# Performance work log

Hardware: AMD Instinct MI355X
Metric: run time of the kernel (lower is better)

Reference implementation:

```python
import jax, jax.numpy as jnp
import numpy as np

HEAD_DIM = 128
MEM_SIZE = 512
MEM_COMPRESS = 256   # mem_size * (1 - hh_keep_rate)
KEEP_HH = 256        # mem_size - mem_compress
LOCAL_LEN = 64


def setup_inputs() -> dict:
    key = jax.random.key(0)
    ks = jax.random.split(key, 8)
    b, h, s, d = 2, 32, 8192, HEAD_DIM
    return dict(
        past_key_states=jax.random.normal(ks[0], (b, h, s, d), jnp.float32),
        past_value_states=jax.random.normal(ks[1], (b, h, s, d), jnp.float32),
        hh_scores=jax.random.uniform(ks[2], (b, h, s), jnp.float32),
        conv0_w=jax.random.normal(ks[3], (2 * MEM_COMPRESS, 2 * HEAD_DIM, 3), jnp.float32) * 0.02,
        conv0_b=jax.random.normal(ks[4], (2 * MEM_COMPRESS,), jnp.float32) * 0.02,
        conv1_w=jax.random.normal(ks[5], (MEM_COMPRESS, 2 * MEM_COMPRESS, 3), jnp.float32) * 0.02,
        conv1_b=jax.random.normal(ks[6], (MEM_COMPRESS,), jnp.float32) * 0.02,
        normalizer=jnp.ones((1,), jnp.float32) * 0.5,
    )


def _conv1d(x, w, bias):
    # x: [N, C_in, L], w: [C_out, C_in, K], 'same' padding for K=3
    y = jax.lax.conv_general_dilated(x, w, window_strides=(1,), padding=[(1, 1)],
                                     dimension_numbers=('NCH', 'OIH', 'NCH'))
    return y + bias[None, :, None]


def reference(past_key_states, past_value_states, hh_scores,
              conv0_w, conv0_b, conv1_w, conv1_b, normalizer):
    b, h, s, d = past_key_states.shape
    # ---- partition_past_key_values: topk + scatter mask, then ordered gather
    k_top = KEEP_HH - LOCAL_LEN
    _, hh_idxs = jax.lax.top_k(hh_scores[..., : s - LOCAL_LEN], k_top)  # [b,h,k_top]
    mask = jnp.zeros((b, h, s), dtype=bool)
    bi = jnp.arange(b)[:, None, None]
    hi = jnp.arange(h)[None, :, None]
    mask = mask.at[bi, hi, hh_idxs].set(True)
    mask = mask.at[..., -LOCAL_LEN:].set(True)
    # stable argsort of ~mask puts mask-True positions first, each group in
    # original sequence order == torch.masked_select ordering
    order = jnp.argsort(~mask, axis=-1, stable=True)          # [b,h,s]
    hh_pos = order[..., :KEEP_HH]                              # [b,h,KEEP_HH]
    non_pos = order[..., KEEP_HH:]                             # [b,h,s-KEEP_HH]
    hh_k = jnp.take_along_axis(past_key_states, hh_pos[..., None], axis=2)
    hh_v = jnp.take_along_axis(past_value_states, hh_pos[..., None], axis=2)
    non_k = jnp.take_along_axis(past_key_states, non_pos[..., None], axis=2)
    non_v = jnp.take_along_axis(past_value_states, non_pos[..., None], axis=2)
    non_scores = jnp.take_along_axis(hh_scores, non_pos, axis=-1)  # [b,h,S']
    sp = s - KEEP_HH
    # ---- make_residual_weight: topk -> sorted idx -> scatter ones
    _, ridx = jax.lax.top_k(non_scores, MEM_COMPRESS)
    ridx = jnp.sort(ridx, axis=-1)
    residual = jax.nn.one_hot(ridx, sp, dtype=past_key_states.dtype)  # [b,h,M,S']
    # ---- conv stack over concatenated (K,V) channels
    x = jnp.concatenate([non_k, non_v], axis=-1)               # [b,h,S',2d]
    x = x.transpose(0, 1, 3, 2).reshape(b * h, 2 * d, sp)      # [(b h), 2d, S']
    x = jax.nn.silu(_conv1d(x, conv0_w, conv0_b))
    x = jax.nn.silu(_conv1d(x, conv1_w, conv1_b))              # [(b h), M, S']
    w = jax.nn.softmax(x, axis=-1).reshape(b, h, MEM_COMPRESS, sp)
    w = residual * (1.0 - normalizer) + w * normalizer         # normalizer: [1]
    merged_k = jnp.einsum('bhms,bhsd->bhmd', w, non_k)
    merged_v = jnp.einsum('bhms,bhsd->bhmd', w, non_v)
    keys = jnp.concatenate([hh_k, merged_k], axis=2)           # [b,h,mem_size,d]
    vals = jnp.concatenate([hh_v, merged_v], axis=2)
    return (keys, vals)
```

## Files before the change

### kernel.cpp

```cpp
#include <hip/hip_runtime.h>
#include <stdint.h>

#define BB 2
#define HH 32
#define NBH 64
#define S 8192
#define DD 128
#define SP 7936
#define MC 256
#define KEEP 256
#define LOC 64
#define KTOP 192
#define N1 8128
#define OC0 512
#define IC0 256
#define KK0 768
#define OC1 256
#define IC1 512
#define KK1 1536
#define KEYS_TOTAL ((size_t)NBH * 512 * DD)

typedef unsigned short u16;
typedef __attribute__((ext_vector_type(2))) unsigned short us2;
typedef __attribute__((ext_vector_type(4))) unsigned short us4;
typedef __attribute__((ext_vector_type(8))) unsigned short us8;
typedef __attribute__((ext_vector_type(8))) short bfrag;
typedef __attribute__((ext_vector_type(4))) float ffrag;

__device__ __forceinline__ u16 f2bf(float x) {
  uint32_t u = __float_as_uint(x);
  return (u16)((u + 0x7FFFu + ((u >> 16) & 1u)) >> 16);
}
__device__ __forceinline__ float bf2f(u16 h) {
  return __uint_as_float(((uint32_t)h) << 16);
}

__device__ __forceinline__ void gl_lds16(const u16* g, u16* l) {
  __builtin_amdgcn_global_load_lds(
      (const __attribute__((address_space(1))) void*)g,
      (__attribute__((address_space(3))) void*)l,
      16, 0, 0);
}

__global__ __launch_bounds__(256) void sel_kernel(
    const float* __restrict__ scores, int bh0,
    int* __restrict__ non_pos_g, int* __restrict__ hh_pos_g, int* __restrict__ rpos_g,
    float* __restrict__ sums_g)
{
  __shared__ uint32_t keys[N1];
  __shared__ u16 nonpos_l[SP];
  __shared__ uint32_t hist[256];
  __shared__ int scanb[256];
  __shared__ uint32_t s_pref, s_pmask;
  __shared__ int s_krem;

  const int slot = blockIdx.x;
  const int bh = bh0 + slot;
  const int tid = threadIdx.x;
  const float* row = scores + (size_t)bh * S;

  sums_g[slot * MC + tid] = 0.0f;

  for (int i = tid; i < N1; i += 256) {
    uint32_t u = __float_as_uint(row[i]);
    keys[i] = (u >> 31) ? ~u : (u | 0x80000000u);
  }
  __syncthreads();

  if (tid == 0) { s_pref = 0; s_pmask = 0; s_krem = KTOP; }
  __syncthreads();
  for (int shift = 24; shift >= 0; shift -= 8) {
    hist[tid] = 0; __syncthreads();
    uint32_t pm = s_pmask, pf = s_pref;
    for (int i = tid; i < N1; i += 256) {
      uint32_t u = keys[i];
      if ((u & pm) == pf) atomicAdd(&hist[(u >> shift) & 255u], 1u);
    }
    __syncthreads();
    if (tid == 0) {
      int krem = s_krem, c = 0, chosen = 0;
      for (int b = 255; b >= 0; --b) {
        int h = (int)hist[b];
        if (krem <= c + h) { chosen = b; krem -= c; break; }
        c += h;
      }
      s_pref |= ((uint32_t)chosen) << shift;
      s_pmask |= 255u << shift;
      s_krem = krem;
    }
    __syncthreads();
  }
  const uint32_t T1 = s_pref;
  const int need1 = s_krem;

  const int base = tid * 32;
  int eqc = 0;
  for (int j = 0; j < 32; ++j) { int i = base + j; if (i < N1 && keys[i] == T1) ++eqc; }
  __syncthreads(); scanb[tid] = eqc; __syncthreads();
  if (tid == 0) { int run = 0; for (int t = 0; t < 256; ++t) { int v = scanb[t]; scanb[t] = run; run += v; } }
  __syncthreads();
  const int eqb = scanb[tid];

  int mcnt = 0;
  { int er = eqb;
    for (int j = 0; j < 32; ++j) {
      int i = base + j; bool m;
      if (i >= N1) m = true;
      else { uint32_t u = keys[i];
        if (u > T1) m = true; else if (u == T1) { m = (er < need1); ++er; } else m = false; }
      if (m) ++mcnt;
    } }
  __syncthreads(); scanb[tid] = mcnt; __syncthreads();
  if (tid == 0) { int run = 0; for (int t = 0; t < 256; ++t) { int v = scanb[t]; scanb[t] = run; run += v; } }
  __syncthreads();
  { int mo = scanb[tid];
    int no = base - mo;
    int er = eqb;
    for (int j = 0; j < 32; ++j) {
      int i = base + j; bool m;
      if (i >= N1) m = true;
      else { uint32_t u = keys[i];
        if (u > T1) m = true; else if (u == T1) { m = (er < need1); ++er; } else m = false; }
      if (m) { hh_pos_g[slot * KEEP + mo] = i; ++mo; }
      else   { nonpos_l[no] = (u16)i; non_pos_g[(size_t)slot * SP + no] = i; ++no; }
    } }
  __syncthreads();

  if (tid == 0) { s_pref = 0; s_pmask = 0; s_krem = MC; }
  __syncthreads();
  for (int shift = 24; shift >= 0; shift -= 8) {
    hist[tid] = 0; __syncthreads();
    uint32_t pm = s_pmask, pf = s_pref;
    for (int i = tid; i < SP; i += 256) {
      uint32_t u = keys[nonpos_l[i]];
      if ((u & pm) == pf) atomicAdd(&hist[(u >> shift) & 255u], 1u);
    }
    __syncthreads();
    if (tid == 0) {
      int krem = s_krem, c = 0, chosen = 0;
      for (int b = 255; b >= 0; --b) {
        int h = (int)hist[b];
        if (krem <= c + h) { chosen = b; krem -= c; break; }
        c += h;
      }
      s_pref |= ((uint32_t)chosen) << shift;
      s_pmask |= 255u << shift;
      s_krem = krem;
    }
    __syncthreads();
  }
  const uint32_t T2 = s_pref;
  const int need2 = s_krem;
  const int b2 = tid * 31;
  int eqc2 = 0;
  for (int j = 0; j < 31; ++j) { if (keys[nonpos_l[b2 + j]] == T2) ++eqc2; }
  __syncthreads(); scanb[tid] = eqc2; __syncthreads();
  if (tid == 0) { int run = 0; for (int t = 0; t < 256; ++t) { int v = scanb[t]; scanb[t] = run; run += v; } }
  __syncthreads();
  const int eqb2 = scanb[tid];
  int sc = 0;
  { int er = eqb2;
    for (int j = 0; j < 31; ++j) {
      uint32_t u = keys[nonpos_l[b2 + j]]; bool sel;
      if (u > T2) sel = true; else if (u == T2) { sel = (er < need2); ++er; } else sel = false;
      if (sel) ++sc;
    } }
  __syncthreads(); scanb[tid] = sc; __syncthreads();
  if (tid == 0) { int run = 0; for (int t = 0; t < 256; ++t) { int v = scanb[t]; scanb[t] = run; run += v; } }
  __syncthreads();
  { int so = scanb[tid];
    int er = eqb2;
    for (int j = 0; j < 31; ++j) {
      int i = b2 + j; uint32_t u = keys[nonpos_l[i]]; bool sel;
      if (u > T2) sel = true; else if (u == T2) { sel = (er < need2); ++er; } else sel = false;
      if (sel) { rpos_g[slot * MC + so] = (int)nonpos_l[i]; ++so; }
    } }
}

__global__ __launch_bounds__(256) void gather_kernel(
    const float* __restrict__ pk, const float* __restrict__ pv,
    const int* __restrict__ non_pos, u16* __restrict__ Xtm_all,
    u16* __restrict__ Xdm_all, u16* __restrict__ Y0_all, int bh0)
{
  __shared__ u16 lt[256][66];
  const int slot = blockIdx.y, tile = blockIdx.x;
  const int bh = bh0 + slot;
  const int tid = threadIdx.x, lane = tid & 63, q = tid >> 6;
  const int t0 = tile * 64;
  u16* Xtm = Xtm_all + (size_t)slot * (SP + 2) * 256 + 256;
  const int* np = non_pos + (size_t)slot * SP;

  for (int r = q; r < 64; r += 4) {
    const int t = t0 + r;
    const int pos = np[t];
    float2 kk = ((const float2*)(pk + ((size_t)bh * S + pos) * DD))[lane];
    float2 vv = ((const float2*)(pv + ((size_t)bh * S + pos) * DD))[lane];
    u16 k0 = f2bf(kk.x), k1 = f2bf(kk.y), v0 = f2bf(vv.x), v1 = f2bf(vv.y);
    us2 tk = {k0, k1}; us2 tv = {v0, v1};
    *(us2*)&Xtm[(size_t)t * 256 + lane * 2] = tk;
    *(us2*)&Xtm[(size_t)t * 256 + 128 + lane * 2] = tv;
    lt[lane * 2][r] = k0; lt[lane * 2 + 1][r] = k1;
    lt[128 + lane * 2][r] = v0; lt[128 + lane * 2 + 1][r] = v1;
  }
  if (tile == 0) {
    Xtm[-256 + tid] = 0;
    u16* y0 = Y0_all + (size_t)slot * (SP + 2) * 512;
    y0[tid] = 0; y0[tid + 256] = 0;
  } else if (tile == 123) {
    Xtm[(size_t)SP * 256 + tid] = 0;
    u16* y0 = Y0_all + (size_t)slot * (SP + 2) * 512 + (size_t)(SP + 1) * 512;
    y0[tid] = 0; y0[tid + 256] = 0;
  }
  __syncthreads();
  u16* Xdm = Xdm_all + (size_t)slot * 256 * SP;
  for (int idx = tid; idx < 4096; idx += 256) {
    const int r = idx >> 4, j = idx & 15;
    uint2 v = *(const uint2*)&lt[r][j * 4];
    *(uint2*)(Xdm + (size_t)r * SP + t0 + j * 4) = v;
  }
}

__global__ __launch_bounds__(256) void hhgather_kernel(
    const float* __restrict__ pk, const float* __restrict__ pv,
    const int* __restrict__ hh_pos, float* __restrict__ out, int bh0)
{
  const int slot = blockIdx.y, bh = bh0 + slot;
  const int tid = threadIdx.x, lane = tid & 63, q = tid >> 6;
  const int r0 = blockIdx.x * 16;
  const int* hp = hh_pos + slot * KEEP;
  for (int r = r0 + q; r < r0 + 16; r += 4) {
    const int pos = hp[r];
    float2 kk = ((const float2*)(pk + ((size_t)bh * S + pos) * DD))[lane];
    float2 vv = ((const float2*)(pv + ((size_t)bh * S + pos) * DD))[lane];
    ((float2*)(out + ((size_t)bh * 512 + r) * DD))[lane] = kk;
    ((float2*)(out + KEYS_TOTAL + ((size_t)bh * 512 + r) * DD))[lane] = vv;
  }
}

__global__ __launch_bounds__(256) void prepack_kernel(
    const float* __restrict__ w0, const float* __restrict__ w1,
    u16* __restrict__ A0, u16* __restrict__ A1)
{
  const int idx = blockIdx.x * 256 + threadIdx.x;
  if (idx < OC0 * KK0) {
    int oc = idx / KK0, r = idx % KK0, tau = r / IC0, ic = r % IC0;
    A0[idx] = f2bf(w0[(oc * IC0 + ic) * 3 + tau]);
  }
  if (idx < OC1 * KK1) {
    int oc = idx / KK1, r = idx % KK1, tau = r / IC1, ic = r % IC1;
    A1[idx] = f2bf(w1[(oc * IC1 + ic) * 3 + tau]);
  }
}

template<int MTOT, int KTOT, int TAUCH, int OUTMODE>
__global__ __launch_bounds__(256) void conv_gemm_kernel(
    const u16* __restrict__ Apack, const u16* __restrict__ Bsrc_all,
    const float* __restrict__ bias, u16* __restrict__ out_all,
    float* __restrict__ sums_g)
{
  __shared__ u16 smem[128 * 136];
  __shared__ float rowsum[128];
  u16* Asl = smem;
  u16* Bsl = smem + 4096;
  const int slot = blockIdx.z;
  const int m0 = blockIdx.y * 128;
  const int t0 = blockIdx.x * 128;
  const int tid = threadIdx.x;
  const int lane = tid & 63, wave = tid >> 6;
  const int wm = (wave & 1) * 64, wn = (wave >> 1) * 64;
  const int r_fr = lane & 15, quad = lane >> 4;
  const u16* Bsrc = Bsrc_all + (size_t)slot * (size_t)(SP + 2) * TAUCH + TAUCH;

  ffrag acc[4][4];
  #pragma unroll
  for (int a = 0; a < 4; ++a)
    #pragma unroll
    for (int b = 0; b < 4; ++b) acc[a][b] = (ffrag)0.0f;

  const int c0 = wave * 2;
  const int lrow = lane >> 2, lcol = (lane & 3) * 8;
  const u16* gA0 = Apack + (size_t)(m0 + c0 * 16 + lrow) * KTOT + lcol;
  const u16* gA1 = gA0 + (size_t)16 * KTOT;
  const u16* gB0 = Bsrc + ((long)t0 + c0 * 16 + lrow - 1) * (long)TAUCH + lcol;
  const u16* gB1 = gB0 + (size_t)16 * TAUCH;
  u16* lA = Asl + c0 * 512;
  u16* lB = Bsl + c0 * 512;

  for (int kt = 0; kt < KTOT / 32; ++kt) {
    const int ko = kt * 32;
    __syncthreads();
    gl_lds16(gA0 + ko, lA);
    gl_lds16(gA1 + ko, lA + 512);
    gl_lds16(gB0 + ko, lB);
    gl_lds16(gB1 + ko, lB + 512);
    __syncthreads();
    bfrag af[4], bf[4];
    #pragma unroll
    for (int mt = 0; mt < 4; ++mt)
      af[mt] = *(const bfrag*)&Asl[(wm + mt * 16 + r_fr) * 32 + quad * 8];
    #pragma unroll
    for (int nt = 0; nt < 4; ++nt)
      bf[nt] = *(const bfrag*)&Bsl[(wn + nt * 16 + r_fr) * 32 + quad * 8];
    #pragma unroll
    for (int mt = 0; mt < 4; ++mt)
      #pragma unroll
      for (int nt = 0; nt < 4; ++nt)
        acc[mt][nt] = __builtin_amdgcn_mfma_f32_16x16x32_bf16(af[mt], bf[nt], acc[mt][nt], 0, 0, 0);
  }
  __syncthreads();
  if constexpr (OUTMODE == 1) {
    if (tid < 128) rowsum[tid] = 0.0f;
    __syncthreads();
  }

  #pragma unroll
  for (int mt = 0; mt < 4; ++mt) {
    float srow4[4] = {0.0f, 0.0f, 0.0f, 0.0f};
    #pragma unroll
    for (int nt = 0; nt < 4; ++nt) {
      const int n_l = wn + nt * 16 + r_fr;
      const int m_l = wm + mt * 16 + quad * 4;
      if constexpr (OUTMODE == 0) {
        u16 h4[4];
        #pragma unroll
        for (int r = 0; r < 4; ++r) {
          float x = acc[mt][nt][r] + bias[m0 + m_l + r];
          float y = x / (1.0f + __expf(-x));
          h4[r] = f2bf(y);
        }
        us4 p = {h4[0], h4[1], h4[2], h4[3]};
        *(us4*)&smem[n_l * 136 + m_l] = p;
      } else {
        #pragma unroll
        for (int r = 0; r < 4; ++r) {
          float x = acc[mt][nt][r] + bias[m0 + m_l + r];
          float y = x / (1.0f + __expf(-x));
          float p = __expf(fminf(y, 60.0f));
          srow4[r] += p;
          smem[(m_l + r) * 136 + n_l] = f2bf(p);
        }
      }
    }
    if constexpr (OUTMODE == 1) {
      #pragma unroll
      for (int r = 0; r < 4; ++r) {
        float s = srow4[r];
        s += __shfl_xor(s, 1, 64);
        s += __shfl_xor(s, 2, 64);
        s += __shfl_xor(s, 4, 64);
        s += __shfl_xor(s, 8, 64);
        if ((lane & 15) == 0)
          atomicAdd(&rowsum[wm + mt * 16 + quad * 4 + r], s);
      }
    }
  }
  __syncthreads();
  if constexpr (OUTMODE == 1) {
    if (tid < 128) atomicAdd(&sums_g[slot * MC + m0 + tid], rowsum[tid]);
  }
  const int rr = tid >> 1, half = tid & 1;
  if (OUTMODE == 0) {
    u16* orow = out_all + (size_t)slot * (size_t)(SP + 2) * MTOT + MTOT
              + (size_t)(t0 + rr) * MTOT + m0 + half * 64;
    const u16* srcr = &smem[rr * 136 + half * 64];
    #pragma unroll
    for (int j = 0; j < 8; ++j) *(us8*)(orow + j * 8) = *(const us8*)(srcr + j * 8);
  } else {
    u16* orow = out_all + (size_t)slot * (size_t)MC * SP
              + (size_t)(m0 + rr) * SP + t0 + half * 64;
    const u16* srcr = &smem[rr * 136 + half * 64];
    #pragma unroll
    for (int j = 0; j < 8; ++j) *(us8*)(orow + j * 8) = *(const us8*)(srcr + j * 8);
  }
}

__global__ __launch_bounds__(256) void gemm3_kernel(
    const u16* __restrict__ Wmm_all, const u16* __restrict__ Xdm_all,
    float* __restrict__ part)
{
  __shared__ u16 smem[8192];
  u16* Asl = smem;
  u16* Bsl = smem + 4096;
  const int kc = blockIdx.x;
  const int tile = blockIdx.y;
  const int slot = blockIdx.z;
  const int m0 = (tile >> 1) * 128, n0 = (tile & 1) * 128;
  const int tid = threadIdx.x;
  const int lane = tid & 63, wave = tid >> 6;
  const int wm = (wave & 1) * 64, wn = (wave >> 1) * 64;
  const int r_fr = lane & 15, quad = lane >> 4;
  const u16* A = Wmm_all + (size_t)slot * MC * SP;
  const u16* Bt = Xdm_all + (size_t)slot * 256 * SP;
  const int kbeg = kc * (SP / 4);

  ffrag acc[4][4];
  #pragma unroll
  for (int a = 0; a < 4; ++a)
    #pragma unroll
    for (int b = 0; b < 4; ++b) acc[a][b] = (ffrag)0.0f;

  const int c0 = wave * 2;
  const int lrow = lane >> 2, lcol = (lane & 3) * 8;
  const u16* gA0 = A + (size_t)(m0 + c0 * 16 + lrow) * SP + kbeg + lcol;
  const u16* gA1 = gA0 + (size_t)16 * SP;
  const u16* gB0 = Bt + (size_t)(n0 + c0 * 16 + lrow) * SP + kbeg + lcol;
  const u16* gB1 = gB0 + (size_t)16 * SP;
  u16* lA = Asl + c0 * 512;
  u16* lB = Bsl + c0 * 512;

  for (int kt = 0; kt < (SP / 4) / 32; ++kt) {
    const int ko = kt * 32;
    __syncthreads();
    gl_lds16(gA0 + ko, lA);
    gl_lds16(gA1 + ko, lA + 512);
    gl_lds16(gB0 + ko, lB);
    gl_lds16(gB1 + ko, lB + 512);
    __syncthreads();
    bfrag af[4], bf[4];
    #pragma unroll
    for (int mt = 0; mt < 4; ++mt)
      af[mt] = *(const bfrag*)&Asl[(wm + mt * 16 + r_fr) * 32 + quad * 8];
    #pragma unroll
    for (int nt = 0; nt < 4; ++nt)
      bf[nt] = *(const bfrag*)&Bsl[(wn + nt * 16 + r_fr) * 32 + quad * 8];
    #pragma unroll
    for (int mt = 0; mt < 4; ++mt)
      #pragma unroll
      for (int nt = 0; nt < 4; ++nt)
        acc[mt][nt] = __builtin_amdgcn_mfma_f32_16x16x32_bf16(af[mt], bf[nt], acc[mt][nt], 0, 0, 0);
  }
  float* pbase = part + ((size_t)slot * 4 + kc) * MC * 256;
  #pragma unroll
  for (int mt = 0; mt < 4; ++mt)
    #pragma unroll
    for (int nt = 0; nt < 4; ++nt) {
      const int n_l = wn + nt * 16 + r_fr;
      const int m_l = wm + mt * 16 + quad * 4;
      #pragma unroll
      for (int r = 0; r < 4; ++r)
        pbase[(size_t)(m0 + m_l + r) * 256 + n0 + n_l] = acc[mt][nt][r];
    }
}

__global__ __launch_bounds__(256) void combine_kernel(
    const float* __restrict__ part, const float* __restrict__ pk, const float* __restrict__ pv,
    const int* __restrict__ rpos, const float* __restrict__ nrmp,
    const float* __restrict__ sums_g, float* __restrict__ out, int bh0)
{
  const int slot = blockIdx.y;
  const int m = blockIdx.x * 4 + (threadIdx.x >> 6);
  const int lane = threadIdx.x & 63;
  const int bh = bh0 + slot;
  const float nrm = nrmp[0];
  const float rw = 1.0f - nrm;
  const float scale = nrm / sums_g[slot * MC + m];
  const int pos = rpos[slot * MC + m];
  const float* krow = pk + ((size_t)bh * S + pos) * DD;
  const float* vrow = pv + ((size_t)bh * S + pos) * DD;
  const size_t pb = (size_t)slot * 4 * MC * 256;
  #pragma unroll
  for (int h = 0; h < 2; ++h) {
    const int d = lane + h * 64;
    float sk = 0.0f, sv = 0.0f;
    #pragma unroll
    for (int kcc = 0; kcc < 4; ++kcc) {
      const float* pp = part + pb + (size_t)kcc * MC * 256 + (size_t)m * 256;
      sk += pp[d];
      sv += pp[128 + d];
    }
    sk = sk * scale + rw * krow[d];
    sv = sv * scale + rw * vrow[d];
    out[((size_t)bh * 512 + KEEP + m) * DD + d] = sk;
    out[KEYS_TOTAL + ((size_t)bh * 512 + KEEP + m) * DD + d] = sv;
  }
}

extern "C" void kernel_launch(void* const* d_in, const int* in_sizes, int n_in,
                              void* d_out, int out_size, void* d_ws, size_t ws_size,
                              hipStream_t stream)
{
  (void)in_sizes; (void)n_in; (void)out_size;
  const float* pk = (const float*)d_in[0];
  const float* pv = (const float*)d_in[1];
  const float* scores = (const float*)d_in[2];
  const float* w0 = (const float*)d_in[3];
  const float* b0 = (const float*)d_in[4];
  const float* w1 = (const float*)d_in[5];
  const float* b1 = (const float*)d_in[6];
  const float* nrmp = (const float*)d_in[7];
  float* out = (float*)d_out;
  char* ws = (char*)d_ws;

  auto alignup = [](size_t x) { return (x + 255) & ~(size_t)255; };
  const size_t offA0 = 0;
  const size_t offA1 = alignup(offA0 + (size_t)OC0 * KK0 * 2);
  const size_t fixed_end = alignup(offA1 + (size_t)OC1 * KK1 * 2);

  const size_t sz_np = (size_t)SP * 4;
  const size_t sz_hh = (size_t)KEEP * 4;
  const size_t sz_rp = (size_t)MC * 4;
  const size_t sz_sm = (size_t)MC * 4;
  const size_t sz_xtm = (size_t)(SP + 2) * 256 * 2;
  const size_t sz_xdm = (size_t)256 * SP * 2;
  const size_t sz_y0 = (size_t)(SP + 2) * 512 * 2;
  const size_t sz_w = (size_t)MC * SP * 2;
  const size_t sz_part = (size_t)4 * MC * 256 * 4;

  auto need_for = [&](int g) -> size_t {
    size_t o = fixed_end;
    o = alignup(o + (size_t)g * sz_np);
    o = alignup(o + (size_t)g * sz_hh);
    o = alignup(o + (size_t)g * sz_rp);
    o = alignup(o + (size_t)g * sz_sm);
    o = alignup(o + (size_t)g * sz_xtm);
    o = alignup(o + (size_t)g * sz_xdm);
    o = alignup(o + (size_t)g * sz_y0);
    o = alignup(o + (size_t)g * sz_w);
    o = alignup(o + (size_t)g * sz_part);
    return o;
  };
  int G = 1;
  const int cand[7] = {64, 32, 16, 8, 4, 2, 1};
  for (int ci = 0; ci < 7; ++ci) { if (need_for(cand[ci]) <= ws_size) { G = cand[ci]; break; } }

  size_t o = fixed_end;
  const size_t off_np = o;  o = alignup(o + (size_t)G * sz_np);
  const size_t off_hh = o;  o = alignup(o + (size_t)G * sz_hh);
  const size_t off_rp = o;  o = alignup(o + (size_t)G * sz_rp);
  const size_t off_sm = o;  o = alignup(o + (size_t)G * sz_sm);
  const size_t off_xtm = o; o = alignup(o + (size_t)G * sz_xtm);
  const size_t off_xdm = o; o = alignup(o + (size_t)G * sz_xdm);
  const size_t off_y0 = o;  o = alignup(o + (size_t)G * sz_y0);
  const size_t off_w = o;   o = alignup(o + (size_t)G * sz_w);
  const size_t off_part = o;

  u16* A0 = (u16*)(ws + offA0);
  u16* A1 = (u16*)(ws + offA1);
  int* np_p = (int*)(ws + off_np);
  int* hh_p = (int*)(ws + off_hh);
  int* rp_p = (int*)(ws + off_rp);
  float* sums = (float*)(ws + off_sm);
  u16* Xtm = (u16*)(ws + off_xtm);
  u16* Xdm = (u16*)(ws + off_xdm);
  u16* Y0 = (u16*)(ws + off_y0);
  u16* Wmm = (u16*)(ws + off_w);
  float* part = (float*)(ws + off_part);

  prepack_kernel<<<1536, 256, 0, stream>>>(w0, w1, A0, A1);

  for (int bh0 = 0; bh0 < NBH; bh0 += G) {
    sel_kernel<<<G, 256, 0, stream>>>(scores, bh0, np_p, hh_p, rp_p, sums);
    gather_kernel<<<dim3(124, G), 256, 0, stream>>>(pk, pv, np_p, Xtm, Xdm, Y0, bh0);
    hhgather_kernel<<<dim3(16, G), 256, 0, stream>>>(pk, pv, hh_p, out, bh0);
    conv_gemm_kernel<OC0, KK0, 256, 0><<<dim3(62, 4, G), 256, 0, stream>>>(A0, Xtm, b0, Y0, sums);
    conv_gemm_kernel<OC1, KK1, 512, 1><<<dim3(62, 2, G), 256, 0, stream>>>(A1, Y0, b1, Wmm, sums);
    gemm3_kernel<<<dim3(4, 4, G), 256, 0, stream>>>(Wmm, Xdm, part);
    combine_kernel<<<dim3(64, G), 256, 0, stream>>>(part, pk, pv, rp_p, nrmp, sums, out, bh0);
  }
}
```

Before: 2.393 ms.

## Double-buffer LDS tiles in conv and gemm3 kernels and remap blocks across XCDs

Both GEMM-style kernels now use two LDS buffers, so the global-to-LDS load for the next K-step is issued before the MFMA work on the current step, and each K-step needs one barrier instead of two. The conv kernels also flatten the grid to 1D and remap block indices so consecutive tiles that share A/B data land on the same XCD, aiming at better L2 reuse. This costs twice the LDS staging in gemm3 and may reduce occupancy there. It relies on NK being even for the paired-loop structure.

```diff
diff --git a/kernel.cpp b/kernel.cpp
--- a/kernel.cpp
+++ b/kernel.cpp
@@ -258,13 +258,22 @@
     const float* __restrict__ bias, u16* __restrict__ out_all,
     float* __restrict__ sums_g)
 {
+  constexpr int MTILES = MTOT / 128;
+  constexpr int NK = KTOT / 32;
+  constexpr int NX = (SP / 128) * MTILES;
+  constexpr int QX = NX / 8, RX = NX % 8;
   __shared__ u16 smem[128 * 136];
   __shared__ float rowsum[128];
-  u16* Asl = smem;
-  u16* Bsl = smem + 4096;
-  const int slot = blockIdx.z;
-  const int m0 = blockIdx.y * 128;
-  const int t0 = blockIdx.x * 128;
+  u16* A0l = smem;
+  u16* A1l = smem + 4096;
+  u16* B0l = smem + 8192;
+  u16* B1l = smem + 12288;
+  const int slot = blockIdx.y;
+  const int lin = blockIdx.x;
+  const int xcd = lin & 7, pos = lin >> 3;
+  const int widx = (xcd < RX ? xcd * (QX + 1) : RX * (QX + 1) + (xcd - RX) * QX) + pos;
+  const int m0 = (widx % MTILES) * 128;
+  const int t0 = (widx / MTILES) * 128;
   const int tid = threadIdx.x;
   const int lane = tid & 63, wave = tid >> 6;
   const int wm = (wave & 1) * 64, wn = (wave >> 1) * 64;
@@ -283,17 +292,10 @@
   const u16* gA1 = gA0 + (size_t)16 * KTOT;
   const u16* gB0 = Bsrc + ((long)t0 + c0 * 16 + lrow - 1) * (long)TAUCH + lcol;
   const u16* gB1 = gB0 + (size_t)16 * TAUCH;
-  u16* lA = Asl + c0 * 512;
-  u16* lB = Bsl + c0 * 512;
-
-  for (int kt = 0; kt < KTOT / 32; ++kt) {
-    const int ko = kt * 32;
-    __syncthreads();
-    gl_lds16(gA0 + ko, lA);
-    gl_lds16(gA1 + ko, lA + 512);
-    gl_lds16(gB0 + ko, lB);
-    gl_lds16(gB1 + ko, lB + 512);
-    __syncthreads();
+  u16* lA0 = A0l + c0 * 512; u16* lA1 = A1l + c0 * 512;
+  u16* lB0 = B0l + c0 * 512; u16* lB1 = B1l + c0 * 512;
+
+  auto compute = [&](const u16* Asl, const u16* Bsl) {
     bfrag af[4], bf[4];
     #pragma unroll
     for (int mt = 0; mt < 4; ++mt)
@@ -306,8 +308,29 @@
       #pragma unroll
       for (int nt = 0; nt < 4; ++nt)
         acc[mt][nt] = __builtin_amdgcn_mfma_f32_16x16x32_bf16(af[mt], bf[nt], acc[mt][nt], 0, 0, 0);
-  }
-  __syncthreads();
+  };
+
+  gl_lds16(gA0, lA0); gl_lds16(gA1, lA0 + 512);
+  gl_lds16(gB0, lB0); gl_lds16(gB1, lB0 + 512);
+  __syncthreads();
+
+  for (int kp = 0; kp < NK / 2; ++kp) {
+    {
+      const int ko = (2 * kp + 1) * 32;
+      gl_lds16(gA0 + ko, lA1); gl_lds16(gA1 + ko, lA1 + 512);
+      gl_lds16(gB0 + ko, lB1); gl_lds16(gB1 + ko, lB1 + 512);
+    }
+    compute(A0l, B0l);
+    __syncthreads();
+    if (2 * kp + 2 < NK) {
+      const int ko = (2 * kp + 2) * 32;
+      gl_lds16(gA0 + ko, lA0); gl_lds16(gA1 + ko, lA0 + 512);
+      gl_lds16(gB0 + ko, lB0); gl_lds16(gB1 + ko, lB0 + 512);
+    }
+    compute(A1l, B1l);
+    __syncthreads();
+  }
+
   if constexpr (OUTMODE == 1) {
     if (tid < 128) rowsum[tid] = 0.0f;
     __syncthreads();
@@ -378,9 +401,11 @@
     const u16* __restrict__ Wmm_all, const u16* __restrict__ Xdm_all,
     float* __restrict__ part)
 {
-  __shared__ u16 smem[8192];
-  u16* Asl = smem;
-  u16* Bsl = smem + 4096;
+  __shared__ u16 smem[16384];
+  u16* A0l = smem;
+  u16* A1l = smem + 4096;
+  u16* B0l = smem + 8192;
+  u16* B1l = smem + 12288;
   const int kc = blockIdx.x;
   const int tile = blockIdx.y;
   const int slot = blockIdx.z;
@@ -392,6 +417,7 @@
   const u16* A = Wmm_all + (size_t)slot * MC * SP;
   const u16* Bt = Xdm_all + (size_t)slot * 256 * SP;
   const int kbeg = kc * (SP / 4);
+  constexpr int NK = (SP / 4) / 32;
 
   ffrag acc[4][4];
   #pragma unroll
@@ -405,17 +431,10 @@
   const u16* gA1 = gA0 + (size_t)16 * SP;
   const u16* gB0 = Bt + (size_t)(n0 + c0 * 16 + lrow) * SP + kbeg + lcol;
   const u16* gB1 = gB0 + (size_t)16 * SP;
-  u16* lA = Asl + c0 * 512;
-  u16* lB = Bsl + c0 * 512;
-
-  for (int kt = 0; kt < (SP / 4) / 32; ++kt) {
-    const int ko = kt * 32;
-    __syncthreads();
-    gl_lds16(gA0 + ko, lA);
-    gl_lds16(gA1 + ko, lA + 512);
-    gl_lds16(gB0 + ko, lB);
-    gl_lds16(gB1 + ko, lB + 512);
-    __syncthreads();
+  u16* lA0 = A0l + c0 * 512; u16* lA1 = A1l + c0 * 512;
+  u16* lB0 = B0l + c0 * 512; u16* lB1 = B1l + c0 * 512;
+
+  auto compute = [&](const u16* Asl, const u16* Bsl) {
     bfrag af[4], bf[4];
     #pragma unroll
     for (int mt = 0; mt < 4; ++mt)
@@ -428,7 +447,29 @@
       #pragma unroll
       for (int nt = 0; nt < 4; ++nt)
         acc[mt][nt] = __builtin_amdgcn_mfma_f32_16x16x32_bf16(af[mt], bf[nt], acc[mt][nt], 0, 0, 0);
-  }
+  };
+
+  gl_lds16(gA0, lA0); gl_lds16(gA1, lA0 + 512);
+  gl_lds16(gB0, lB0); gl_lds16(gB1, lB0 + 512);
+  __syncthreads();
+
+  for (int kp = 0; kp < NK / 2; ++kp) {
+    {
+      const int ko = (2 * kp + 1) * 32;
+      gl_lds16(gA0 + ko, lA1); gl_lds16(gA1 + ko, lA1 + 512);
+      gl_lds16(gB0 + ko, lB1); gl_lds16(gB1 + ko, lB1 + 512);
+    }
+    compute(A0l, B0l);
+    __syncthreads();
+    if (2 * kp + 2 < NK) {
+      const int ko = (2 * kp + 2) * 32;
+      gl_lds16(gA0 + ko, lA0); gl_lds16(gA1 + ko, lA0 + 512);
+      gl_lds16(gB0 + ko, lB0); gl_lds16(gB1 + ko, lB0 + 512);
+    }
+    compute(A1l, B1l);
+    __syncthreads();
+  }
+
   float* pbase = part + ((size_t)slot * 4 + kc) * MC * 256;
   #pragma unroll
   for (int mt = 0; mt < 4; ++mt)
@@ -552,8 +593,8 @@
     sel_kernel<<<G, 256, 0, stream>>>(scores, bh0, np_p, hh_p, rp_p, sums);
     gather_kernel<<<dim3(124, G), 256, 0, stream>>>(pk, pv, np_p, Xtm, Xdm, Y0, bh0);
     hhgather_kernel<<<dim3(16, G), 256, 0, stream>>>(pk, pv, hh_p, out, bh0);
-    conv_gemm_kernel<OC0, KK0, 256, 0><<<dim3(62, 4, G), 256, 0, stream>>>(A0, Xtm, b0, Y0, sums);
-    conv_gemm_kernel<OC1, KK1, 512, 1><<<dim3(62, 2, G), 256, 0, stream>>>(A1, Y0, b1, Wmm, sums);
+    conv_gemm_kernel<OC0, KK0, 256, 0><<<dim3(248, G), 256, 0, stream>>>(A0, Xtm, b0, Y0, sums);
+    conv_gemm_kernel<OC1, KK1, 512, 1><<<dim3(124, G), 256, 0, stream>>>(A1, Y0, b1, Wmm, sums);
     gemm3_kernel<<<dim3(4, 4, G), 256, 0, stream>>>(Wmm, Xdm, part);
     combine_kernel<<<dim3(64, G), 256, 0, stream>>>(part, pk, pv, rp_p, nrmp, sums, out, bh0);
   }
```

Measured after the change: 2.481 ms. 1.04x slower.

## Double K-step per barrier and remap conv GEMM blocks for XCD locality

Applied to the files above, without the earlier changes.

The conv GEMM and gemm3 kernels now load a 64-wide K slice per iteration (two 32-wide halves in LDS), which halves the number of syncthreads barriers per unit of MFMA work. The conv GEMM grid is also flattened and remapped so that consecutive tiles, which share the same time range and M tiles, land on the same XCD under round-robin dispatch, improving L2 reuse of the B operand. LDS use doubles for these tiles, which may lower occupancy.

```diff
diff --git a/kernel.cpp b/kernel.cpp
--- a/kernel.cpp
+++ b/kernel.cpp
@@ -258,13 +258,20 @@
     const float* __restrict__ bias, u16* __restrict__ out_all,
     float* __restrict__ sums_g)
 {
+  constexpr int MTILES = MTOT / 128;
+  constexpr int NK = KTOT / 64;
+  constexpr int NX = (SP / 128) * MTILES;
+  constexpr int QX = NX / 8, RX = NX % 8;
   __shared__ u16 smem[128 * 136];
   __shared__ float rowsum[128];
   u16* Asl = smem;
-  u16* Bsl = smem + 4096;
-  const int slot = blockIdx.z;
-  const int m0 = blockIdx.y * 128;
-  const int t0 = blockIdx.x * 128;
+  u16* Bsl = smem + 8192;
+  const int slot = blockIdx.y;
+  const int lin = blockIdx.x;
+  const int xcd = lin & 7, pos = lin >> 3;
+  const int widx = (xcd < RX ? xcd * (QX + 1) : RX * (QX + 1) + (xcd - RX) * QX) + pos;
+  const int m0 = (widx % MTILES) * 128;
+  const int t0 = (widx / MTILES) * 128;
   const int tid = threadIdx.x;
   const int lane = tid & 63, wave = tid >> 6;
   const int wm = (wave & 1) * 64, wn = (wave >> 1) * 64;
@@ -277,35 +284,39 @@
     #pragma unroll
     for (int b = 0; b < 4; ++b) acc[a][b] = (ffrag)0.0f;
 
-  const int c0 = wave * 2;
   const int lrow = lane >> 2, lcol = (lane & 3) * 8;
-  const u16* gA0 = Apack + (size_t)(m0 + c0 * 16 + lrow) * KTOT + lcol;
-  const u16* gA1 = gA0 + (size_t)16 * KTOT;
-  const u16* gB0 = Bsrc + ((long)t0 + c0 * 16 + lrow - 1) * (long)TAUCH + lcol;
-  const u16* gB1 = gB0 + (size_t)16 * TAUCH;
-  u16* lA = Asl + c0 * 512;
-  u16* lB = Bsl + c0 * 512;
-
-  for (int kt = 0; kt < KTOT / 32; ++kt) {
-    const int ko = kt * 32;
-    __syncthreads();
-    gl_lds16(gA0 + ko, lA);
-    gl_lds16(gA1 + ko, lA + 512);
-    gl_lds16(gB0 + ko, lB);
-    gl_lds16(gB1 + ko, lB + 512);
-    __syncthreads();
-    bfrag af[4], bf[4];
-    #pragma unroll
-    for (int mt = 0; mt < 4; ++mt)
-      af[mt] = *(const bfrag*)&Asl[(wm + mt * 16 + r_fr) * 32 + quad * 8];
-    #pragma unroll
-    for (int nt = 0; nt < 4; ++nt)
-      bf[nt] = *(const bfrag*)&Bsl[(wn + nt * 16 + r_fr) * 32 + quad * 8];
-    #pragma unroll
-    for (int mt = 0; mt < 4; ++mt)
+  const u16* gA = Apack + (size_t)(m0 + wave * 32 + lrow) * KTOT + lcol;
+  const u16* gB = Bsrc + ((long)t0 + wave * 32 + lrow - 1) * (long)TAUCH + lcol;
+  u16* lA = Asl + wave * 1024;
+  u16* lB = Bsl + wave * 1024;
+
+  for (int kt = 0; kt < NK; ++kt) {
+    const int ko = kt * 64;
+    __syncthreads();
+    gl_lds16(gA + ko,                  lA);
+    gl_lds16(gA + ko + 16 * KTOT,      lA + 512);
+    gl_lds16(gA + ko + 32,             lA + 4096);
+    gl_lds16(gA + ko + 32 + 16 * KTOT, lA + 4096 + 512);
+    gl_lds16(gB + ko,                  lB);
+    gl_lds16(gB + ko + 16 * TAUCH,     lB + 512);
+    gl_lds16(gB + ko + 32,             lB + 4096);
+    gl_lds16(gB + ko + 32 + 16 * TAUCH, lB + 4096 + 512);
+    __syncthreads();
+    #pragma unroll
+    for (int kk = 0; kk < 2; ++kk) {
+      bfrag af[4], bf[4];
+      #pragma unroll
+      for (int mt = 0; mt < 4; ++mt)
+        af[mt] = *(const bfrag*)&Asl[kk * 4096 + (wm + mt * 16 + r_fr) * 32 + quad * 8];
       #pragma unroll
       for (int nt = 0; nt < 4; ++nt)
-        acc[mt][nt] = __builtin_amdgcn_mfma_f32_16x16x32_bf16(af[mt], bf[nt], acc[mt][nt], 0, 0, 0);
+        bf[nt] = *(const bfrag*)&Bsl[kk * 4096 + (wn + nt * 16 + r_fr) * 32 + quad * 8];
+      #pragma unroll
+      for (int mt = 0; mt < 4; ++mt)
+        #pragma unroll
+        for (int nt = 0; nt < 4; ++nt)
+          acc[mt][nt] = __builtin_amdgcn_mfma_f32_16x16x32_bf16(af[mt], bf[nt], acc[mt][nt], 0, 0, 0);
+    }
   }
   __syncthreads();
   if constexpr (OUTMODE == 1) {
@@ -378,9 +389,9 @@
     const u16* __restrict__ Wmm_all, const u16* __restrict__ Xdm_all,
     float* __restrict__ part)
 {
-  __shared__ u16 smem[8192];
+  __shared__ u16 smem[16384];
   u16* Asl = smem;
-  u16* Bsl = smem + 4096;
+  u16* Bsl = smem + 8192;
   const int kc = blockIdx.x;
   const int tile = blockIdx.y;
   const int slot = blockIdx.z;
@@ -392,6 +403,7 @@
   const u16* A = Wmm_all + (size_t)slot * MC * SP;
   const u16* Bt = Xdm_all + (size_t)slot * 256 * SP;
   const int kbeg = kc * (SP / 4);
+  constexpr int NK = (SP / 4) / 64;
 
   ffrag acc[4][4];
   #pragma unroll
@@ -399,36 +411,41 @@
     #pragma unroll
     for (int b = 0; b < 4; ++b) acc[a][b] = (ffrag)0.0f;
 
-  const int c0 = wave * 2;
   const int lrow = lane >> 2, lcol = (lane & 3) * 8;
-  const u16* gA0 = A + (size_t)(m0 + c0 * 16 + lrow) * SP + kbeg + lcol;
-  const u16* gA1 = gA0 + (size_t)16 * SP;
-  const u16* gB0 = Bt + (size_t)(n0 + c0 * 16 + lrow) * SP + kbeg + lcol;
-  const u16* gB1 = gB0 + (size_t)16 * SP;
-  u16* lA = Asl + c0 * 512;
-  u16* lB = Bsl + c0 * 512;
-
-  for (int kt = 0; kt < (SP / 4) / 32; ++kt) {
-    const int ko = kt * 32;
-    __syncthreads();
-    gl_lds16(gA0 + ko, lA);
-    gl_lds16(gA1 + ko, lA + 512);
-    gl_lds16(gB0 + ko, lB);
-    gl_lds16(gB1 + ko, lB + 512);
-    __syncthreads();
-    bfrag af[4], bf[4];
-    #pragma unroll
-    for (int mt = 0; mt < 4; ++mt)
-      af[mt] = *(const bfrag*)&Asl[(wm + mt * 16 + r_fr) * 32 + quad * 8];
-    #pragma unroll
-    for (int nt = 0; nt < 4; ++nt)
-      bf[nt] = *(const bfrag*)&Bsl[(wn + nt * 16 + r_fr) * 32 + quad * 8];
-    #pragma unroll
-    for (int mt = 0; mt < 4; ++mt)
+  const u16* gA = A + (size_t)(m0 + wave * 32 + lrow) * SP + kbeg + lcol;
+  const u16* gB = Bt + (size_t)(n0 + wave * 32 + lrow) * SP + kbeg + lcol;
+  u16* lA = Asl + wave * 1024;
+  u16* lB = Bsl + wave * 1024;
+
+  for (int kt = 0; kt < NK; ++kt) {
+    const int ko = kt * 64;
+    __syncthreads();
+    gl_lds16(gA + ko,                lA);
+    gl_lds16(gA + ko + 16 * SP,      lA + 512);
+    gl_lds16(gA + ko + 32,           lA + 4096);
+    gl_lds16(gA + ko + 32 + 16 * SP, lA + 4096 + 512);
+    gl_lds16(gB + ko,                lB);
+    gl_lds16(gB + ko + 16 * SP,      lB + 512);
+    gl_lds16(gB + ko + 32,           lB + 4096);
+    gl_lds16(gB + ko + 32 + 16 * SP, lB + 4096 + 512);
+    __syncthreads();
+    #pragma unroll
+    for (int kk = 0; kk < 2; ++kk) {
+      bfrag af[4], bf[4];
+      #pragma unroll
+      for (int mt = 0; mt < 4; ++mt)
+        af[mt] = *(const bfrag*)&Asl[kk * 4096 + (wm + mt * 16 + r_fr) * 32 + quad * 8];
       #pragma unroll
       for (int nt = 0; nt < 4; ++nt)
-        acc[mt][nt] = __builtin_amdgcn_mfma_f32_16x16x32_bf16(af[mt], bf[nt], acc[mt][nt], 0, 0, 0);
-  }
+        bf[nt] = *(const bfrag*)&Bsl[kk * 4096 + (wn + nt * 16 + r_fr) * 32 + quad * 8];
+      #pragma unroll
+      for (int mt = 0; mt < 4; ++mt)
+        #pragma unroll
+        for (int nt = 0; nt < 4; ++nt)
+          acc[mt][nt] = __builtin_amdgcn_mfma_f32_16x16x32_bf16(af[mt], bf[nt], acc[mt][nt], 0, 0, 0);
+    }
+  }
+
   float* pbase = part + ((size_t)slot * 4 + kc) * MC * 256;
   #pragma unroll
   for (int mt = 0; mt < 4; ++mt)
@@ -552,8 +569,8 @@
     sel_kernel<<<G, 256, 0, stream>>>(scores, bh0, np_p, hh_p, rp_p, sums);
     gather_kernel<<<dim3(124, G), 256, 0, stream>>>(pk, pv, np_p, Xtm, Xdm, Y0, bh0);
     hhgather_kernel<<<dim3(16, G), 256, 0, stream>>>(pk, pv, hh_p, out, bh0);
-    conv_gemm_kernel<OC0, KK0, 256, 0><<<dim3(62, 4, G), 256, 0, stream>>>(A0, Xtm, b0, Y0, sums);
-    conv_gemm_kernel<OC1, KK1, 512, 1><<<dim3(62, 2, G), 256, 0, stream>>>(A1, Y0, b1, Wmm, sums);
+    conv_gemm_kernel<OC0, KK0, 256, 0><<<dim3(248, G), 256, 0, stream>>>(A0, Xtm, b0, Y0, sums);
+    conv_gemm_kernel<OC1, KK1, 512, 1><<<dim3(124, G), 256, 0, stream>>>(A1, Y0, b1, Wmm, sums);
     gemm3_kernel<<<dim3(4, 4, G), 256, 0, stream>>>(Wmm, Xdm, part);
     combine_kernel<<<dim3(64, G), 256, 0, stream>>>(part, pk, pv, rp_p, nrmp, sums, out, bh0);
   }
```

Result: no change. 2.365 ms (-1.2%).
